# Optimization experiments

Measured on AMD Instinct MI355X. Metric: run time of the kernel, lower is better.

Reference implementation:

```python
import jax, jax.numpy as jnp
import numpy as np

B, N, M = 4, 2048, 2048
DIM, DIM_KEYS, DIM_OUT = 512, 512, 512
HEADS, DIM_HEAD = 8, 64
INNER = HEADS * DIM_HEAD


def setup_inputs() -> dict:
    key = jax.random.key(0)
    ks = jax.random.split(key, 9)
    x = jax.random.normal(ks[0], (B, N, DIM), dtype=jnp.float32)
    context = jax.random.normal(ks[1], (B, M, DIM_KEYS), dtype=jnp.float32)
    mask = jax.random.randint(ks[2], (B, N), 0, 2).astype(bool)
    context_mask = jax.random.randint(ks[3], (B, M), 0, 2).astype(bool)
    Wq = jax.random.normal(ks[4], (DIM, INNER), dtype=jnp.float32) * 0.02
    Wkv = jax.random.normal(ks[5], (DIM_KEYS, 2 * INNER), dtype=jnp.float32) * 0.02
    Wo = jax.random.normal(ks[6], (INNER, DIM_OUT), dtype=jnp.float32) * 0.02
    bo = jnp.zeros((DIM_OUT,), dtype=jnp.float32)
    null_key = jax.random.normal(ks[7], (DIM_HEAD,), dtype=jnp.float32)
    null_value = jax.random.normal(ks[8], (DIM_HEAD,), dtype=jnp.float32)
    return {"x": x, "context": context, "mask": mask, "context_mask": context_mask,
            "Wq": Wq, "Wkv": Wkv, "Wo": Wo, "bo": bo,
            "null_key": null_key, "null_value": null_value}


def reference(x, context, mask, context_mask, Wq, Wkv, Wo, bo, null_key, null_value):
    b, n, _ = x.shape
    m = context.shape[1]
    h, dh = HEADS, DIM_HEAD
    scale = dh ** -0.5

    # projections -> [b, h, n, dh]
    q = (x @ Wq).reshape(b, n, h, dh).transpose(0, 2, 1, 3)
    kv = context @ Wkv  # [b, m, 2*inner]
    k, v = jnp.split(kv, 2, axis=-1)
    k = k.reshape(b, m, h, dh).transpose(0, 2, 1, 3)
    v = v.reshape(b, m, h, dh).transpose(0, 2, 1, 3)

    # prepend null key/value token -> j = m + 1
    nk = jnp.broadcast_to(null_key, (b, h, 1, dh))
    nv = jnp.broadcast_to(null_value, (b, h, 1, dh))
    k = jnp.concatenate([nk, k], axis=2)
    v = jnp.concatenate([nv, v], axis=2)

    # qk activation (tanh) BEFORE the dot product
    q = jnp.tanh(q)
    k = jnp.tanh(k)

    sim = jnp.einsum('bhid,bhjd->bhij', q, k) * scale  # [b,h,n,m+1]

    # null token is always attendable -> pad context mask with True
    cm = jnp.pad(context_mask, ((0, 0), (1, 0)), constant_values=True)
    full_mask = mask[:, None, :, None] & cm[:, None, None, :]
    neg = -jnp.finfo(sim.dtype).max
    sim = jnp.where(full_mask, sim, neg)

    attn = jax.nn.softmax(sim, axis=-1)
    out = jnp.einsum('bhij,bhjd->bhid', attn, v)
    out = out.transpose(0, 2, 1, 3).reshape(b, n, h * dh)
    return out @ Wo + bo
```

## Files before the change

kernel.cpp:

```cpp
#include <hip/hip_runtime.h>
#include <math.h>

#define BB 4
#define NN 2048
#define MM 2048
#define HEADS 8
#define DH 64

typedef _Float16 f16;
typedef _Float16 f16x4 __attribute__((ext_vector_type(4)));
typedef _Float16 f16x8 __attribute__((ext_vector_type(8)));
typedef float f32x4 __attribute__((ext_vector_type(4)));
typedef unsigned short ushort;

#define LOG2E 1.44269504088896f
#define QSCALE (0.125f * LOG2E)

#if __has_builtin(__builtin_amdgcn_exp2f)
#define EXP2(x) __builtin_amdgcn_exp2f(x)
#else
#define EXP2(x) exp2f(x)
#endif

__device__ __forceinline__ f16x4 pk4(float a, float b, float c, float d) {
#if __has_builtin(__builtin_amdgcn_cvt_pkrtz)
    auto t0 = __builtin_amdgcn_cvt_pkrtz(a, b);
    auto t1 = __builtin_amdgcn_cvt_pkrtz(c, d);
    f16x4 r;
    r[0] = t0[0]; r[1] = t0[1]; r[2] = t1[0]; r[3] = t1[1];
    return r;
#else
    f16x4 r = {(f16)a, (f16)b, (f16)c, (f16)d};
    return r;
#endif
}

__device__ __forceinline__ void gl16(const void* g, void* l) {
    __builtin_amdgcn_global_load_lds(
        (const __attribute__((address_space(1))) unsigned int*)g,
        (__attribute__((address_space(3))) unsigned int*)l, 16, 0, 0);
}

__global__ void wprep_k(const float* __restrict__ Wq, const float* __restrict__ Wkv,
                        const float* __restrict__ Wo,
                        f16* __restrict__ wq16, f16* __restrict__ wkv16,
                        f16* __restrict__ woh, f16* __restrict__ wol)
{
    __shared__ f16 S0[64 * 36], S1[64 * 36];
    const int tid = threadIdx.x;
    const int bid = blockIdx.x;
    const int K = 512;
    const float* W; int N; f16* T16; f16 *Th, *Tl; int id;
    if (bid < 128)      { W = Wq;  N = 512;  T16 = wq16;  Th = 0; Tl = 0; id = bid; }
    else if (bid < 384) { W = Wkv; N = 1024; T16 = wkv16; Th = 0; Tl = 0; id = bid - 128; }
    else                { W = Wo;  N = 512;  T16 = 0; Th = woh; Tl = wol; id = bid - 384; }
    const int k0 = (id & 15) * 32, n0 = (id >> 4) * 64;
    const int kr = tid >> 3, nc = (tid & 7) * 8;
    float4 v0 = *(const float4*)(W + (size_t)(k0 + kr) * N + n0 + nc);
    float4 v1 = *(const float4*)(W + (size_t)(k0 + kr) * N + n0 + nc + 4);
    float e[8] = {v0.x, v0.y, v0.z, v0.w, v1.x, v1.y, v1.z, v1.w};
    const int n = tid >> 2, kc = (tid & 3) * 8;
    if (T16) {
#pragma unroll
        for (int j = 0; j < 8; j++) S0[(nc + j) * 36 + kr] = (f16)e[j];
        __syncthreads();
        *(uint4*)(T16 + (size_t)(n0 + n) * K + k0 + kc) = *(const uint4*)(S0 + n * 36 + kc);
    } else {
#pragma unroll
        for (int j = 0; j < 8; j++) {
            f16 h = (f16)e[j];
            S0[(nc + j) * 36 + kr] = h;
            S1[(nc + j) * 36 + kr] = (f16)(e[j] - (float)h);
        }
        __syncthreads();
        *(uint4*)(Th + (size_t)(n0 + n) * K + k0 + kc) = *(const uint4*)(S0 + n * 36 + kc);
        *(uint4*)(Tl + (size_t)(n0 + n) * K + k0 + kc) = *(const uint4*)(S1 + n * 36 + kc);
    }
}

__launch_bounds__(256, 3)
__global__ void proj_k(const float* __restrict__ x, const float* __restrict__ ctx,
                       const f16* __restrict__ wq16, const f16* __restrict__ wkv16,
                       f16* __restrict__ qws, f16* __restrict__ kws, f16* __restrict__ vt)
{
    __shared__ __align__(16) char smem[49152];

    const int tid  = threadIdx.x;
    const int wave = tid >> 6, lane = tid & 63;
    const int l15  = lane & 15, quad = lane >> 4;
    const int by = blockIdx.y;
    const int isQ = (by < 4);
    const float* A32 = isQ ? x : ctx;
    const f16* Bt  = isQ ? wq16 : wkv16;
    const int c0 = (isQ ? by : by - 4) * 128;
    const size_t r0 = (size_t)blockIdx.x * 128;
    const int K = 512;

    const int alr = lane >> 3;
    const int asw = (lane & 7) ^ alr;
    const char* aP = (const char*)(A32 + (r0 + wave * 32 + alr) * K) + asw * 16;
    const int blr = lane >> 2;
    const int bsw = (lane & 3) ^ ((lane >> 3) & 3);
    const char* bP = (const char*)(Bt + (size_t)(c0 + wave * 32 + blr) * K) + bsw * 16;
    char* aD = smem + wave * 4096;
    char* bD = smem + 16384 + wave * 2048;

    gl16(aP,          aD);
    gl16(aP + 16384,  aD + 1024);
    gl16(aP + 32768,  aD + 2048);
    gl16(aP + 49152,  aD + 3072);
    gl16(bP,          bD);
    gl16(bP + 16384,  bD + 1024);
    aP += 128; bP += 64;

    const int ax  = l15 & 7;
    const int fsw = ((quad ^ ((l15 >> 1) & 3)) << 4);
    const int arow0 = (wave * 32 + l15) * 128;
    const int ac0 = (((2 * quad) ^ ax) << 4);

    f32x4 acc[2][8] = {};
    __syncthreads();

    int buf = 0;
    for (int t = 0; t < 16; t++) {
        const int nb = (buf ^ 1) * 24576;
        if (t < 15) {
            gl16(aP,          aD + nb);
            gl16(aP + 16384,  aD + nb + 1024);
            gl16(aP + 32768,  aD + nb + 2048);
            gl16(aP + 49152,  aD + nb + 3072);
            gl16(bP,          bD + nb);
            gl16(bP + 16384,  bD + nb + 1024);
            aP += 128; bP += 64;
        }
        const char* sA = smem + buf * 24576;
        const char* sB = sA + 16384;

        f16x8 a[2];
#pragma unroll
        for (int rt = 0; rt < 2; rt++) {
            const int ab = arow0 + rt * 2048;
            f32x4 lo = *(const f32x4*)(sA + ab + ac0);
            f32x4 hi = *(const f32x4*)(sA + ab + (ac0 ^ 16));
            a[rt][0] = (f16)lo[0]; a[rt][1] = (f16)lo[1];
            a[rt][2] = (f16)lo[2]; a[rt][3] = (f16)lo[3];
            a[rt][4] = (f16)hi[0]; a[rt][5] = (f16)hi[1];
            a[rt][6] = (f16)hi[2]; a[rt][7] = (f16)hi[3];
        }
#pragma unroll
        for (int half = 0; half < 2; half++) {
            f16x8 b[4];
#pragma unroll
            for (int c = 0; c < 4; c++)
                b[c] = *(const f16x8*)(sB + ((half * 4 + c) * 16 + l15) * 64 + fsw);
#pragma unroll
            for (int rt = 0; rt < 2; rt++)
#pragma unroll
                for (int c = 0; c < 4; c++)
                    acc[rt][half * 4 + c] = __builtin_amdgcn_mfma_f32_16x16x32_f16(
                        a[rt], b[c], acc[rt][half * 4 + c], 0, 0, 0);
        }
        __syncthreads();
        buf ^= 1;
    }

    const int b    = (int)(r0 >> 11);
    const int rloc = ((int)(r0 & 2047)) + wave * 32;

#pragma unroll
    for (int rt = 0; rt < 2; rt++)
#pragma unroll
        for (int ct = 0; ct < 8; ct++) {
            const int col = c0 + ct * 16 + l15;
            if (isQ || col < 512) {
                const int h = (col >> 6) & 7;
                const int d = col & 63;
                f16* dst = isQ ? qws : kws;
                const float sc = isQ ? QSCALE : 1.0f;
#pragma unroll
                for (int reg = 0; reg < 4; reg++) {
                    const int nn = rloc + rt * 16 + quad * 4 + reg;
                    dst[(((size_t)b * 8 + h) * 2048 + nn) * 64 + d] =
                        (f16)(tanhf(acc[rt][ct][reg]) * sc);
                }
            } else {
                const int c = col - 512;
                const int h = c >> 6;
                const int d = c & 63;
                const int m0 = rloc + rt * 16 + quad * 4;
                f16x4 pk;
#pragma unroll
                for (int reg = 0; reg < 4; reg++) pk[reg] = (f16)acc[rt][ct][reg];
                *(f16x4*)(vt + (((size_t)b * 8 + h) * 64 + d) * 2048 + m0) = pk;
            }
        }
}

__launch_bounds__(256, 4)
__global__ void attn_k(const f16* __restrict__ qws, const f16* __restrict__ kws,
                       const f16* __restrict__ vtws,
                       const int* __restrict__ mask, const int* __restrict__ cmask,
                       const float* __restrict__ nk, const float* __restrict__ nv,
                       f16* __restrict__ Opf, float* __restrict__ lp)
{
    __shared__ __align__(16) char smem[32768];

    const int tid  = threadIdx.x;
    const int wave = tid >> 6, lane = tid & 63;
    const int l15  = lane & 15, quad = lane >> 4;
    const int bh = blockIdx.x, b = bh >> 3, h = bh & 7;
    const int q0 = blockIdx.y * 128 + wave * 32;
    const int jh = blockIdx.z;
    const int jbeg = jh << 9, jend = jbeg + 512;

    const f16* kg0 = kws + (size_t)bh * MM * DH;
    const f16* vg0 = vtws + (size_t)bh * DH * MM;

    const int lrow = lane >> 3;
    const int lsw  = ((lane & 7) ^ lrow) << 4;
    const char* kP = (const char*)kg0 + (size_t)(jbeg + wave * 16 + lrow) * 128 + lsw;
    const char* vP = (const char*)vg0 + (size_t)(wave * 16 + lrow) * 4096
                   + (size_t)jbeg * 2 + lsw;
    char* kD = smem + wave * 2048;
    char* vD = smem + 8192 + wave * 2048;

    gl16(kP,         kD);
    gl16(kP + 1024,  kD + 1024);
    gl16(vP,         vD);
    gl16(vP + 32768, vD + 1024);
    kP += 8192; vP += 128;

    f16x8 qf[2][2];
    const f16* qbase = qws + ((size_t)bh * NN + q0) * DH;
#pragma unroll
    for (int rt = 0; rt < 2; rt++)
#pragma unroll
        for (int ks = 0; ks < 2; ks++)
            qf[rt][ks] = *(const f16x8*)(qbase + (rt * 16 + l15) * DH + ks * 32 + quad * 8);

    int rowOk[2];
#pragma unroll
    for (int rt = 0; rt < 2; rt++)
        rowOk[rt] = mask[(size_t)b * NN + q0 + rt * 16 + l15];

    float pnull[2] = {0.0f, 0.0f};
    if (jh == 0) {
        float pn[2] = {0.f, 0.f};
#pragma unroll
        for (int ks = 0; ks < 2; ks++)
#pragma unroll
            for (int t = 0; t < 8; t++) {
                const float nkt = tanhf(nk[ks * 32 + quad * 8 + t]);
                pn[0] += (float)qf[0][ks][t] * nkt;
                pn[1] += (float)qf[1][ks][t] * nkt;
            }
#pragma unroll
        for (int rt = 0; rt < 2; rt++) {
            pn[rt] += __shfl_xor(pn[rt], 16);
            pn[rt] += __shfl_xor(pn[rt], 32);
            pnull[rt] = rowOk[rt] ? EXP2(pn[rt]) : 1.0f;
        }
    }
    float negsel[2];
#pragma unroll
    for (int rt = 0; rt < 2; rt++) {
        negsel[rt] = rowOk[rt] ? -1.0e30f : 0.0f;
        if (!rowOk[rt]) {
            const f16x8 zz = {(f16)0, (f16)0, (f16)0, (f16)0, (f16)0, (f16)0, (f16)0, (f16)0};
            qf[rt][0] = zz; qf[rt][1] = zz;
        }
    }

    f32x4 acc[2][4];
    f32x4 accl[2];
#pragma unroll
    for (int rt = 0; rt < 2; rt++)
#pragma unroll
        for (int reg = 0; reg < 4; reg++) {
            const float pr = __shfl(pnull[rt], quad * 4 + reg, 16);
            accl[rt][reg] = pr;
#pragma unroll
            for (int ds = 0; ds < 4; ds++)
                acc[rt][ds][reg] = pr * nv[ds * 16 + l15];
        }

    const f16x4 vone = {(f16)1, (f16)1, (f16)1, (f16)1};
    const int kxor = l15 & 7;

    __syncthreads();

    int buf = 0;
    for (int jc = jbeg; jc < jend; jc += 64) {
        int4 cmv[4];
#pragma unroll
        for (int jj = 0; jj < 4; jj++)
            cmv[jj] = *(const int4*)(cmask + (size_t)b * MM + jc + jj * 16 + quad * 4);

        if (jc + 64 < jend) {
            const int bo = (buf ^ 1) << 14;
            gl16(kP,         kD + bo);
            gl16(kP + 1024,  kD + bo + 1024);
            gl16(vP,         vD + bo);
            gl16(vP + 32768, vD + bo + 1024);
            kP += 8192; vP += 128;
        }

        const char* sKb = smem + (buf << 14);
        const char* sVb = sKb + 8192;

        f32x4 st[2][4];
#pragma unroll
        for (int rt = 0; rt < 2; rt++)
#pragma unroll
            for (int jj = 0; jj < 4; jj++) {
                st[rt][jj][0] = cmv[jj].x ? 0.0f : negsel[rt];
                st[rt][jj][1] = cmv[jj].y ? 0.0f : negsel[rt];
                st[rt][jj][2] = cmv[jj].z ? 0.0f : negsel[rt];
                st[rt][jj][3] = cmv[jj].w ? 0.0f : negsel[rt];
            }

#pragma unroll
        for (int ks = 0; ks < 2; ks++) {
            f16x8 kb[4];
#pragma unroll
            for (int jj = 0; jj < 4; jj++)
                kb[jj] = *(const f16x8*)(sKb + (jj * 16 + l15) * 128
                                             + (((ks * 4 + quad) ^ kxor) << 4));
#pragma unroll
            for (int rt = 0; rt < 2; rt++)
#pragma unroll
                for (int jj = 0; jj < 4; jj++)
                    st[rt][jj] = __builtin_amdgcn_mfma_f32_16x16x32_f16(
                        kb[jj], qf[rt][ks], st[rt][jj], 0, 0, 0);
        }

        f16x4 pa[2][4];
#pragma unroll
        for (int rt = 0; rt < 2; rt++)
#pragma unroll
            for (int jj = 0; jj < 4; jj++)
                pa[rt][jj] = pk4(EXP2(st[rt][jj][0]), EXP2(st[rt][jj][1]),
                                 EXP2(st[rt][jj][2]), EXP2(st[rt][jj][3]));

#pragma unroll
        for (int jj = 0; jj < 4; jj++) {
            f16x4 vb[4];
#pragma unroll
            for (int ds = 0; ds < 4; ds++)
                vb[ds] = *(const f16x4*)(sVb + (ds * 16 + l15) * 128
                                             + (((jj * 2 + (quad >> 1)) ^ kxor) << 4)
                                             + ((quad & 1) << 3));
#pragma unroll
            for (int rt = 0; rt < 2; rt++) {
#pragma unroll
                for (int ds = 0; ds < 4; ds++)
                    acc[rt][ds] = __builtin_amdgcn_mfma_f32_16x16x16f16(
                        pa[rt][jj], vb[ds], acc[rt][ds], 0, 0, 0);
                accl[rt] = __builtin_amdgcn_mfma_f32_16x16x16f16(
                    pa[rt][jj], vone, accl[rt], 0, 0, 0);
            }
        }

        __syncthreads();
        buf ^= 1;
    }

#pragma unroll
    for (int rt = 0; rt < 2; rt++) {
        float inv[4];
#pragma unroll
        for (int reg = 0; reg < 4; reg++)
            inv[reg] = 1.0f / fmaxf(accl[rt][reg], 1e-35f);
#pragma unroll
        for (int ds = 0; ds < 4; ds++)
#pragma unroll
            for (int reg = 0; reg < 4; reg++) {
                const int r = q0 + rt * 16 + quad * 4 + reg;
                Opf[((size_t)jh * 8192 + b * 2048 + r) * 512 + h * 64 + ds * 16 + l15] =
                    (f16)(acc[rt][ds][reg] * inv[reg]);
            }
    }
    if (l15 == 0) {
#pragma unroll
        for (int rt = 0; rt < 2; rt++)
#pragma unroll
            for (int reg = 0; reg < 4; reg++)
                lp[((size_t)jh * 32 + bh) * 2048 + q0 + rt * 16 + quad * 4 + reg] =
                    accl[rt][reg];
    }
}

__global__ void merge_k(const f16* __restrict__ Opf, const float* __restrict__ lp,
                        f16* __restrict__ of16)
{
    const int i = blockIdx.x * 256 + threadIdx.x;
    const int row = i >> 7;
    const int c4  = i & 127;
    const int b = row >> 11, n = row & 2047, h = c4 >> 4;
    float w[4], den = 0.f;
#pragma unroll
    for (int jh = 0; jh < 4; jh++) {
        w[jh] = lp[((size_t)jh * 32 + b * 8 + h) * 2048 + n];
        den += w[jh];
    }
    const float inv = 1.0f / den;
    float v0 = 0, v1 = 0, v2 = 0, v3 = 0;
#pragma unroll
    for (int jh = 0; jh < 4; jh++) {
        f16x4 o = *(const f16x4*)(Opf + ((size_t)jh * 8192 + row) * 512 + c4 * 4);
        v0 += (float)o[0] * w[jh];
        v1 += (float)o[1] * w[jh];
        v2 += (float)o[2] * w[jh];
        v3 += (float)o[3] * w[jh];
    }
    f16x4 r = pk4(v0 * inv, v1 * inv, v2 * inv, v3 * inv);
    *(f16x4*)(of16 + (size_t)row * 512 + c4 * 4) = r;
}

__launch_bounds__(256, 4)
__global__ void mgemm2(const f16* __restrict__ A, const f16* __restrict__ Bh,
                       const f16* __restrict__ Bl,
                       float* __restrict__ o32, const float* __restrict__ bias,
                       int K)
{
    __shared__ __align__(16) char smem[32768];

    const int tid  = threadIdx.x;
    const int wave = tid >> 6, lane = tid & 63;
    const int l15  = lane & 15, quad = lane >> 4;
    const size_t r0 = (size_t)blockIdx.x * 128;
    const int c0 = blockIdx.y * 64;

    const int blr = lane >> 2;
    const int bsw = (lane & 3) ^ ((lane >> 3) & 3);
    const char* aP = (const char*)(A + (r0 + wave * 32 + blr) * K) + bsw * 16;
    const char* hP = (const char*)(Bh + (size_t)(c0 + wave * 16 + blr) * K) + bsw * 16;
    const char* lP = (const char*)(Bl + (size_t)(c0 + wave * 16 + blr) * K) + bsw * 16;
    char* aD = smem + wave * 2048;
    char* hD = smem + 8192 + wave * 1024;
    char* lD = smem + 12288 + wave * 1024;

    gl16(aP,          aD);
    gl16(aP + 16384,  aD + 1024);
    gl16(hP,          hD);
    gl16(lP,          lD);
    aP += 64; hP += 64; lP += 64;

    const int fsw = ((quad ^ ((l15 >> 1) & 3)) << 4);
    const int aoff0 = (wave * 32 + l15) * 64 + fsw;
    const int aoff1 = aoff0 + 16 * 64;

    f32x4 acc[2][4] = {};
    __syncthreads();

    int buf = 0;
    const int NT = K / 32;
    for (int t = 0; t < NT; t++) {
        const int nb = (buf ^ 1) * 16384;
        if (t < NT - 1) {
            gl16(aP,          aD + nb);
            gl16(aP + 16384,  aD + nb + 1024);
            gl16(hP,          hD + nb);
            gl16(lP,          lD + nb);
            aP += 64; hP += 64; lP += 64;
        }
        const char* sA = smem + buf * 16384;
        const char* sH = sA + 8192;
        const char* sL = sA + 12288;

        f16x8 a[2];
        a[0] = *(const f16x8*)(sA + aoff0);
        a[1] = *(const f16x8*)(sA + aoff1);
#pragma unroll
        for (int ct = 0; ct < 4; ct++) {
            const int boff = (ct * 16 + l15) * 64 + fsw;
            f16x8 bh = *(const f16x8*)(sH + boff);
            f16x8 bl = *(const f16x8*)(sL + boff);
#pragma unroll
            for (int rt = 0; rt < 2; rt++) {
                acc[rt][ct] = __builtin_amdgcn_mfma_f32_16x16x32_f16(
                    a[rt], bh, acc[rt][ct], 0, 0, 0);
                acc[rt][ct] = __builtin_amdgcn_mfma_f32_16x16x32_f16(
                    a[rt], bl, acc[rt][ct], 0, 0, 0);
            }
        }
        __syncthreads();
        buf ^= 1;
    }

#pragma unroll
    for (int rt = 0; rt < 2; rt++)
#pragma unroll
        for (int ct = 0; ct < 4; ct++) {
            const int col = c0 + ct * 16 + l15;
            const float bv = bias[col];
#pragma unroll
            for (int reg = 0; reg < 4; reg++) {
                const size_t row = r0 + wave * 32 + rt * 16 + quad * 4 + reg;
                o32[row * 512 + col] = acc[rt][ct][reg] + bv;
            }
        }
}

extern "C" void kernel_launch(void* const* d_in, const int* in_sizes, int n_in,
                              void* d_out, int out_size, void* d_ws, size_t ws_size,
                              hipStream_t stream)
{
    const float* x    = (const float*)d_in[0];
    const float* ctx  = (const float*)d_in[1];
    const int*   mask = (const int*)d_in[2];
    const int*   cmsk = (const int*)d_in[3];
    const float* Wq   = (const float*)d_in[4];
    const float* Wkv  = (const float*)d_in[5];
    const float* Wo   = (const float*)d_in[6];
    const float* bo   = (const float*)d_in[7];
    const float* nk   = (const float*)d_in[8];
    const float* nv   = (const float*)d_in[9];
    float* out = (float*)d_out;

    const size_t S = (size_t)BB * HEADS * NN * DH;

    f16* qws = (f16*)d_ws;
    f16* kws = qws + S;
    f16* vt  = kws + S;
    f16* wq16  = vt + S;
    f16* wkv16 = wq16 + 512 * 512;
    f16* woh = wkv16 + 512 * 1024;
    f16* wol = woh + 512 * 512;
    float* lp = (float*)(wol + 512 * 512);
    f16* Opf = (f16*)(lp + 4 * 32 * 2048);
    f16* of16 = qws;

    wprep_k<<<512, 256, 0, stream>>>(Wq, Wkv, Wo, wq16, wkv16, woh, wol);
    proj_k<<<dim3(64, 12), 256, 0, stream>>>(x, ctx, wq16, wkv16, qws, kws, vt);
    attn_k<<<dim3(32, 16, 4), 256, 0, stream>>>(qws, kws, vt, mask, cmsk, nk, nv, Opf, lp);
    merge_k<<<4096, 256, 0, stream>>>(Opf, lp, of16);
    mgemm2<<<dim3(64, 8), 256, 0, stream>>>(of16, woh, wol, out, bo, 512);
}
```

Measured before the change: 190.1 us.

## Load GEMM A operands directly into registers instead of staging through LDS

In both the projection GEMM and the output GEMM, the A-operand tiles are no longer copied into shared memory with global_load_lds. Each lane now loads its own A fragment straight from global memory into registers, one k-step ahead, while only the weight (B) tiles stay double-buffered in LDS. This shrinks shared memory per block and removes the LDS reads for A, which could raise occupancy and cut LDS traffic. The cost is redundant and less coalesced global reads of A across waves, and the barrier moves to the top of each loop iteration.

Measured after the change: 206.2 us. 1.08x slower.

```diff
diff --git a/kernel.cpp b/kernel.cpp
--- a/kernel.cpp
+++ b/kernel.cpp
@@ -39,6 +39,13 @@
     __builtin_amdgcn_global_load_lds(
         (const __attribute__((address_space(1))) unsigned int*)g,
         (__attribute__((address_space(3))) unsigned int*)l, 16, 0, 0);
+}
+
+__device__ __forceinline__ f16x8 cvt8(float4 lo, float4 hi) {
+    f16x8 r;
+    r[0] = (f16)lo.x; r[1] = (f16)lo.y; r[2] = (f16)lo.z; r[3] = (f16)lo.w;
+    r[4] = (f16)hi.x; r[5] = (f16)hi.y; r[6] = (f16)hi.z; r[7] = (f16)hi.w;
+    return r;
 }
 
 __global__ void wprep_k(const float* __restrict__ Wq, const float* __restrict__ Wkv,
@@ -83,7 +90,7 @@
                        const f16* __restrict__ wq16, const f16* __restrict__ wkv16,
                        f16* __restrict__ qws, f16* __restrict__ kws, f16* __restrict__ vt)
 {
-    __shared__ __align__(16) char smem[49152];
+    __shared__ __align__(16) char smem[16384];
 
     const int tid  = threadIdx.x;
     const int wave = tid >> 6, lane = tid & 63;
@@ -96,57 +103,47 @@
     const size_t r0 = (size_t)blockIdx.x * 128;
     const int K = 512;
 
-    const int alr = lane >> 3;
-    const int asw = (lane & 7) ^ alr;
-    const char* aP = (const char*)(A32 + (r0 + wave * 32 + alr) * K) + asw * 16;
     const int blr = lane >> 2;
     const int bsw = (lane & 3) ^ ((lane >> 3) & 3);
     const char* bP = (const char*)(Bt + (size_t)(c0 + wave * 32 + blr) * K) + bsw * 16;
-    char* aD = smem + wave * 4096;
-    char* bD = smem + 16384 + wave * 2048;
-
-    gl16(aP,          aD);
-    gl16(aP + 16384,  aD + 1024);
-    gl16(aP + 32768,  aD + 2048);
-    gl16(aP + 49152,  aD + 3072);
+    char* bD = smem + wave * 2048;
+
     gl16(bP,          bD);
     gl16(bP + 16384,  bD + 1024);
-    aP += 128; bP += 64;
-
-    const int ax  = l15 & 7;
+    bP += 64;
+
+    const float* aB0 = A32 + (r0 + wave * 32 + l15) * K + quad * 8;
+    const float* aB1 = aB0 + 16 * K;
+    float4 a0lo = *(const float4*)(aB0);
+    float4 a0hi = *(const float4*)(aB0 + 4);
+    float4 a1lo = *(const float4*)(aB1);
+    float4 a1hi = *(const float4*)(aB1 + 4);
+    int ak = 32;
+
     const int fsw = ((quad ^ ((l15 >> 1) & 3)) << 4);
-    const int arow0 = (wave * 32 + l15) * 128;
-    const int ac0 = (((2 * quad) ^ ax) << 4);
 
     f32x4 acc[2][8] = {};
-    __syncthreads();
 
     int buf = 0;
     for (int t = 0; t < 16; t++) {
-        const int nb = (buf ^ 1) * 24576;
+        __syncthreads();
+        const int nb = (buf ^ 1) * 8192;
         if (t < 15) {
-            gl16(aP,          aD + nb);
-            gl16(aP + 16384,  aD + nb + 1024);
-            gl16(aP + 32768,  aD + nb + 2048);
-            gl16(aP + 49152,  aD + nb + 3072);
             gl16(bP,          bD + nb);
             gl16(bP + 16384,  bD + nb + 1024);
-            aP += 128; bP += 64;
-        }
-        const char* sA = smem + buf * 24576;
-        const char* sB = sA + 16384;
-
+            bP += 64;
+        }
         f16x8 a[2];
-#pragma unroll
-        for (int rt = 0; rt < 2; rt++) {
-            const int ab = arow0 + rt * 2048;
-            f32x4 lo = *(const f32x4*)(sA + ab + ac0);
-            f32x4 hi = *(const f32x4*)(sA + ab + (ac0 ^ 16));
-            a[rt][0] = (f16)lo[0]; a[rt][1] = (f16)lo[1];
-            a[rt][2] = (f16)lo[2]; a[rt][3] = (f16)lo[3];
-            a[rt][4] = (f16)hi[0]; a[rt][5] = (f16)hi[1];
-            a[rt][6] = (f16)hi[2]; a[rt][7] = (f16)hi[3];
-        }
+        a[0] = cvt8(a0lo, a0hi);
+        a[1] = cvt8(a1lo, a1hi);
+        if (t < 15) {
+            a0lo = *(const float4*)(aB0 + ak);
+            a0hi = *(const float4*)(aB0 + ak + 4);
+            a1lo = *(const float4*)(aB1 + ak);
+            a1hi = *(const float4*)(aB1 + ak + 4);
+            ak += 32;
+        }
+        const char* sB = smem + buf * 8192;
 #pragma unroll
         for (int half = 0; half < 2; half++) {
             f16x8 b[4];
@@ -160,7 +157,6 @@
                     acc[rt][half * 4 + c] = __builtin_amdgcn_mfma_f32_16x16x32_f16(
                         a[rt], b[c], acc[rt][half * 4 + c], 0, 0, 0);
         }
-        __syncthreads();
         buf ^= 1;
     }
 
@@ -423,7 +419,7 @@
                        float* __restrict__ o32, const float* __restrict__ bias,
                        int K)
 {
-    __shared__ __align__(16) char smem[32768];
+    __shared__ __align__(16) char smem[16384];
 
     const int tid  = threadIdx.x;
     const int wave = tid >> 6, lane = tid & 63;
@@ -433,58 +429,53 @@
 
     const int blr = lane >> 2;
     const int bsw = (lane & 3) ^ ((lane >> 3) & 3);
-    const char* aP = (const char*)(A + (r0 + wave * 32 + blr) * K) + bsw * 16;
     const char* hP = (const char*)(Bh + (size_t)(c0 + wave * 16 + blr) * K) + bsw * 16;
     const char* lP = (const char*)(Bl + (size_t)(c0 + wave * 16 + blr) * K) + bsw * 16;
-    char* aD = smem + wave * 2048;
-    char* hD = smem + 8192 + wave * 1024;
-    char* lD = smem + 12288 + wave * 1024;
-
-    gl16(aP,          aD);
-    gl16(aP + 16384,  aD + 1024);
-    gl16(hP,          hD);
-    gl16(lP,          lD);
-    aP += 64; hP += 64; lP += 64;
+    char* hD = smem + wave * 1024;
+    char* lD = smem + 4096 + wave * 1024;
+
+    gl16(hP, hD);
+    gl16(lP, lD);
+    hP += 64; lP += 64;
+
+    const f16* aB0 = A + (r0 + wave * 32 + l15) * K + quad * 8;
+    const f16* aB1 = aB0 + 16 * K;
+    f16x8 a0 = *(const f16x8*)(aB0);
+    f16x8 a1 = *(const f16x8*)(aB1);
+    int ak = 32;
 
     const int fsw = ((quad ^ ((l15 >> 1) & 3)) << 4);
-    const int aoff0 = (wave * 32 + l15) * 64 + fsw;
-    const int aoff1 = aoff0 + 16 * 64;
 
     f32x4 acc[2][4] = {};
-    __syncthreads();
 
     int buf = 0;
     const int NT = K / 32;
     for (int t = 0; t < NT; t++) {
-        const int nb = (buf ^ 1) * 16384;
+        __syncthreads();
+        const int nb = (buf ^ 1) * 8192;
         if (t < NT - 1) {
-            gl16(aP,          aD + nb);
-            gl16(aP + 16384,  aD + nb + 1024);
-            gl16(hP,          hD + nb);
-            gl16(lP,          lD + nb);
-            aP += 64; hP += 64; lP += 64;
-        }
-        const char* sA = smem + buf * 16384;
-        const char* sH = sA + 8192;
-        const char* sL = sA + 12288;
-
-        f16x8 a[2];
-        a[0] = *(const f16x8*)(sA + aoff0);
-        a[1] = *(const f16x8*)(sA + aoff1);
+            gl16(hP, hD + nb);
+            gl16(lP, lD + nb);
+            hP += 64; lP += 64;
+        }
+        f16x8 ca0 = a0, ca1 = a1;
+        if (t < NT - 1) {
+            a0 = *(const f16x8*)(aB0 + ak);
+            a1 = *(const f16x8*)(aB1 + ak);
+            ak += 32;
+        }
+        const char* sH = smem + buf * 8192;
+        const char* sL = sH + 4096;
 #pragma unroll
         for (int ct = 0; ct < 4; ct++) {
             const int boff = (ct * 16 + l15) * 64 + fsw;
             f16x8 bh = *(const f16x8*)(sH + boff);
             f16x8 bl = *(const f16x8*)(sL + boff);
-#pragma unroll
-            for (int rt = 0; rt < 2; rt++) {
-                acc[rt][ct] = __builtin_amdgcn_mfma_f32_16x16x32_f16(
-                    a[rt], bh, acc[rt][ct], 0, 0, 0);
-                acc[rt][ct] = __builtin_amdgcn_mfma_f32_16x16x32_f16(
-                    a[rt], bl, acc[rt][ct], 0, 0, 0);
-            }
-        }
-        __syncthreads();
+            acc[0][ct] = __builtin_amdgcn_mfma_f32_16x16x32_f16(ca0, bh, acc[0][ct], 0, 0, 0);
+            acc[0][ct] = __builtin_amdgcn_mfma_f32_16x16x32_f16(ca0, bl, acc[0][ct], 0, 0, 0);
+            acc[1][ct] = __builtin_amdgcn_mfma_f32_16x16x32_f16(ca1, bh, acc[1][ct], 0, 0, 0);
+            acc[1][ct] = __builtin_amdgcn_mfma_f32_16x16x32_f16(ca1, bl, acc[1][ct], 0, 0, 0);
+        }
         buf ^= 1;
     }
 
```
